# Kernel tuning notes

Hardware: AMD Instinct MI355X
Metric: run time of the kernel (lower is better)

Reference implementation:

```python
import jax, jax.numpy as jnp
import numpy as np

B, S, D, H = 2, 2048, 1024, 16
DK = D // H


def setup_inputs() -> dict:
    key = jax.random.key(0)
    ks = jax.random.split(key, 11)
    scale = 1.0 / np.sqrt(D)
    inp = {
        'q': jax.random.normal(ks[0], (B, S, D), jnp.float32),
        'k': jax.random.normal(ks[1], (B, S, D), jnp.float32),
        'v': jax.random.normal(ks[2], (B, S, D), jnp.float32),
        'mask': jnp.tril(jnp.ones((S, S), jnp.int32))[None, None],  # [1,1,S,S] causal
        'w_q': jax.random.normal(ks[3], (D, D), jnp.float32) * scale,
        'b_q': jax.random.normal(ks[4], (D,), jnp.float32) * scale,
        'w_k': jax.random.normal(ks[5], (D, D), jnp.float32) * scale,
        'b_k': jax.random.normal(ks[6], (D,), jnp.float32) * scale,
        'w_v': jax.random.normal(ks[7], (D, D), jnp.float32) * scale,
        'b_v': jax.random.normal(ks[8], (D,), jnp.float32) * scale,
        'w_o': jax.random.normal(ks[9], (D, D), jnp.float32) * scale,
        'b_o': jax.random.normal(ks[10], (D,), jnp.float32) * scale,
    }
    return inp


def reference(q, k, v, mask, w_q, b_q, w_k, b_k, w_v, b_v, w_o, b_o):
    # Linear projections (torch Linear: x @ W^T + b; here weights stored as [D_in, D_out])
    query = q @ w_q + b_q  # [B,S,D]
    key_ = k @ w_k + b_k
    value = v @ w_v + b_v
    # split heads -> [B,H,S,DK]
    def split(x):
        return x.reshape(B, S, H, DK).transpose(0, 2, 1, 3)
    qh, kh, vh = split(query), split(key_), split(value)
    scores = jnp.einsum('bhqd,bhkd->bhqk', qh, kh) / jnp.sqrt(jnp.float32(DK))
    scores = jnp.where(mask == 0, jnp.float32(-1e9), scores)
    attn = jax.nn.softmax(scores, axis=-1)  # dropout p=0.0 -> identity
    out = jnp.einsum('bhqk,bhkd->bhqd', attn, vh)  # [B,H,S,DK]
    out = out.transpose(0, 2, 1, 3).reshape(B, S, D)
    return out @ w_o + b_o
```

## Files before the change

kernel.cpp:

```cpp
#include <hip/hip_runtime.h>

typedef unsigned short u16;
typedef unsigned int u32;
typedef __attribute__((ext_vector_type(8))) short short8;
typedef __attribute__((ext_vector_type(4))) float f32x4;
typedef __attribute__((ext_vector_type(4))) float float4v;
typedef __attribute__((ext_vector_type(4))) u16 u16x4;
typedef __attribute__((ext_vector_type(2))) u32 u32x2;

#define DEV static __device__ __forceinline__

static constexpr int S_LEN = 2048;
static constexpr int D_MODEL = 1024;
static constexpr int N_HEADS = 16;
static constexpr int DK = 64;
static constexpr float LOG2E = 1.4426950408889634f;
static constexpr float SM_SHIFT = 12.0f;

#if defined(__has_builtin)
#if __has_builtin(__builtin_amdgcn_exp2f)
#define EXP2(x) __builtin_amdgcn_exp2f(x)
#else
#define EXP2(x) exp2f(x)
#endif
#else
#define EXP2(x) exp2f(x)
#endif

DEV u16 f2bf(float f) {
  u32 u = __builtin_bit_cast(u32, f);
  u32 r = (u + 0x7FFFu + ((u >> 16) & 1u)) >> 16;
  return (u16)r;
}

DEV u32 pk2bf(float lo, float hi) {
  u32 d;
  asm("v_cvt_pk_bf16_f32 %0, %1, %2" : "=v"(d) : "v"(lo), "v"(hi));
  return d;
}

DEV void async16(const void* g, void* l) {
  __builtin_amdgcn_global_load_lds(
      (const __attribute__((address_space(1))) u32*)g,
      (__attribute__((address_space(3))) u32*)l, 16, 0, 0);
}

DEV short8 lds_frag(const u16* tile, int row, int byteInRow) {
  const char* p = (const char*)tile + row * 128 + (byteInRow ^ ((row & 7) << 4));
  return *(const short8*)p;
}

DEV f32x4 mfma16(short8 a, short8 b, f32x4 c) {
  return __builtin_amdgcn_mfma_f32_16x16x32_bf16(a, b, c, 0, 0, 0);
}

__global__ void k_cvt3(const float* __restrict__ q, const float* __restrict__ k,
                       const float* __restrict__ v, u16* __restrict__ xq,
                       u16* __restrict__ xk, u16* __restrict__ xv, int n) {
  const float* src = blockIdx.y == 0 ? q : (blockIdx.y == 1 ? k : v);
  u16* dst = blockIdx.y == 0 ? xq : (blockIdx.y == 1 ? xk : xv);
  int i = (blockIdx.x * blockDim.x + threadIdx.x) * 4;
  int stride = gridDim.x * blockDim.x * 4;
  for (; i < n; i += stride) {
    float4v f = *(const float4v*)(src + i);
    u16x4 o;
    o[0] = f2bf(f[0]); o[1] = f2bf(f[1]); o[2] = f2bf(f[2]); o[3] = f2bf(f[3]);
    *(u16x4*)(dst + i) = o;
  }
}

__global__ void k_twz4(const float* __restrict__ wq, const float* __restrict__ wk,
                       const float* __restrict__ wv, const float* __restrict__ wo,
                       u16* __restrict__ tq, u16* __restrict__ tk,
                       u16* __restrict__ tv, u16* __restrict__ to_) {
  __shared__ u16 t[64][65];
  const int z = blockIdx.z;
  const float* W = z == 0 ? wq : (z == 1 ? wk : (z == 2 ? wv : wo));
  u16* Wt = z == 0 ? tq : (z == 1 ? tk : (z == 2 ? tv : to_));
  const int n0 = blockIdx.x * 64;
  const int k0 = blockIdx.y * 64;
  const int tid = threadIdx.x;
  const int c = tid & 63, r0 = tid >> 6;
#pragma unroll
  for (int j = 0; j < 16; ++j) {
    int r = r0 + j * 4;
    t[r][c] = f2bf(W[(size_t)(k0 + r) * D_MODEL + n0 + c]);
  }
  __syncthreads();
#pragma unroll
  for (int j = 0; j < 16; ++j) {
    int r = r0 + j * 4;
    Wt[(size_t)(n0 + r) * D_MODEL + k0 + c] = t[c][r];
  }
}

__global__ __launch_bounds__(256, 2) void k_gemm3(
    const u16* __restrict__ Xq, const u16* __restrict__ Xk, const u16* __restrict__ Xv,
    const u16* __restrict__ Wtq, const u16* __restrict__ Wtk, const u16* __restrict__ Wtv,
    const float* __restrict__ bq, const float* __restrict__ bk, const float* __restrict__ bv,
    u16* __restrict__ Qh, u16* __restrict__ Kh, u16* __restrict__ Vtp) {
  const int z = blockIdx.z;
  const u16* A = z == 0 ? Xq : (z == 1 ? Xk : Xv);
  const u16* Bt = z == 0 ? Wtq : (z == 1 ? Wtk : Wtv);
  const float* bias = z == 0 ? bq : (z == 1 ? bk : bv);
  u16* obf = z == 0 ? Qh : (z == 1 ? Kh : Vtp);
  const float scale = z == 0 ? 0.125f * LOG2E : 1.0f;

  __shared__ __align__(16) u16 As[128 * 64];
  __shared__ __align__(16) u16 Bs[128 * 64];
  const int tid = threadIdx.x;
  const int lane = tid & 63, w = tid >> 6;
  const int l15 = lane & 15, l4 = lane >> 4;
  const int bm = blockIdx.x * 128, bn = blockIdx.y * 128;
  const int wr = (w >> 1) * 64, wc = (w & 1) * 64;
  const int sr = tid >> 3, sc8 = tid & 7;
  f32x4 acc[4][4] = {};

  for (int k0 = 0; k0 < 1024; k0 += 64) {
    __syncthreads();
#pragma unroll
    for (int j = 0; j < 4; ++j) {
      int row = sr + j * 32;
      int col = (sc8 ^ (row & 7)) << 3;
      async16(A + (size_t)(bm + row) * 1024 + k0 + col, (char*)As + tid * 16 + j * 4096);
      async16(Bt + (size_t)(bn + row) * 1024 + k0 + col, (char*)Bs + tid * 16 + j * 4096);
    }
    __syncthreads();
    short8 af[4][2], bfv[4][2];
#pragma unroll
    for (int mi = 0; mi < 4; ++mi)
#pragma unroll
      for (int kk = 0; kk < 2; ++kk)
        af[mi][kk] = lds_frag(As, wr + mi * 16 + l15, kk * 64 + l4 * 16);
#pragma unroll
    for (int ni = 0; ni < 4; ++ni)
#pragma unroll
      for (int kk = 0; kk < 2; ++kk)
        bfv[ni][kk] = lds_frag(Bs, wc + ni * 16 + l15, kk * 64 + l4 * 16);
#pragma unroll
    for (int kk = 0; kk < 2; ++kk)
#pragma unroll
      for (int mi = 0; mi < 4; ++mi)
#pragma unroll
        for (int ni = 0; ni < 4; ++ni)
          acc[mi][ni] = mfma16(af[mi][kk], bfv[ni][kk], acc[mi][ni]);
  }

#pragma unroll
  for (int mi = 0; mi < 4; ++mi)
#pragma unroll
    for (int ni = 0; ni < 4; ++ni) {
      const int row0 = bm + wr + mi * 16 + l4 * 4;
      const int col = bn + wc + ni * 16 + l15;
      const int h = col >> 6, dk = col & 63;
      const int b = row0 >> 11, s0 = row0 & 2047;
      if (z == 2) {
        u16x4 pk;
#pragma unroll
        for (int r = 0; r < 4; ++r) pk[r] = f2bf(acc[mi][ni][r] + bias[col]);
        *(u16x4*)(obf + ((size_t)((b * N_HEADS + h) * DK + dk)) * S_LEN + s0) = pk;
      } else {
#pragma unroll
        for (int r = 0; r < 4; ++r) {
          float vv = (acc[mi][ni][r] + bias[col]) * scale;
          obf[(((size_t)(b * N_HEADS + h) * S_LEN + s0 + r) << 6) + dk] = f2bf(vv);
        }
      }
    }
}

__global__ __launch_bounds__(256, 2) void k_gemmO(
    const u16* __restrict__ A, const u16* __restrict__ Bt,
    const float* __restrict__ bias, float* __restrict__ ofp) {
  __shared__ __align__(16) u16 As[128 * 64];
  __shared__ __align__(16) u16 Bs[64 * 64];
  const int tid = threadIdx.x;
  const int lane = tid & 63, w = tid >> 6;
  const int l15 = lane & 15, l4 = lane >> 4;
  const int bm = blockIdx.x * 128, bn = blockIdx.y * 64;
  const int wr = w * 32;
  const int sr = tid >> 3, sc8 = tid & 7;
  f32x4 acc[2][4] = {};

  for (int k0 = 0; k0 < 1024; k0 += 64) {
    __syncthreads();
#pragma unroll
    for (int j = 0; j < 4; ++j) {
      int row = sr + j * 32;
      int col = (sc8 ^ (row & 7)) << 3;
      async16(A + (size_t)(bm + row) * 1024 + k0 + col, (char*)As + tid * 16 + j * 4096);
      if (j < 2)
        async16(Bt + (size_t)(bn + row) * 1024 + k0 + col, (char*)Bs + tid * 16 + j * 4096);
    }
    __syncthreads();
    short8 af[2][2], bfv[4][2];
#pragma unroll
    for (int mi = 0; mi < 2; ++mi)
#pragma unroll
      for (int kk = 0; kk < 2; ++kk)
        af[mi][kk] = lds_frag(As, wr + mi * 16 + l15, kk * 64 + l4 * 16);
#pragma unroll
    for (int ni = 0; ni < 4; ++ni)
#pragma unroll
      for (int kk = 0; kk < 2; ++kk)
        bfv[ni][kk] = lds_frag(Bs, ni * 16 + l15, kk * 64 + l4 * 16);
#pragma unroll
    for (int kk = 0; kk < 2; ++kk)
#pragma unroll
      for (int mi = 0; mi < 2; ++mi)
#pragma unroll
        for (int ni = 0; ni < 4; ++ni)
          acc[mi][ni] = mfma16(af[mi][kk], bfv[ni][kk], acc[mi][ni]);
  }

#pragma unroll
  for (int mi = 0; mi < 2; ++mi)
#pragma unroll
    for (int ni = 0; ni < 4; ++ni)
#pragma unroll
      for (int r = 0; r < 4; ++r) {
        int row = bm + wr + mi * 16 + l4 * 4 + r;
        int col = bn + ni * 16 + l15;
        ofp[(size_t)row * D_MODEL + col] = acc[mi][ni][r] + bias[col];
      }
}

__global__ __launch_bounds__(512, 6) void k_attn(
    const u16* __restrict__ Qh, const u16* __restrict__ Kh,
    const u16* __restrict__ Vt, u16* __restrict__ Om,
    float* __restrict__ Po, float* __restrict__ Pl) {
  __shared__ __align__(16) u16 Ks[2][64 * 64];
  __shared__ __align__(16) u16 Vs[2][64 * 64];
  __shared__ __align__(16) u16 Ps[8][16 * 64];
  const int tid = threadIdx.x;
  const int lane = tid & 63, w = tid >> 6;
  const int l15 = lane & 15, l4 = lane >> 4;
  const int bid = blockIdx.x;

  int bh, g, c, tbeg, tend;
  bool partial;
  if (bid < 256) {
    bh = bid & 31; g = 8 + (bid >> 5); c = 0; tbeg = 0; tend = 16; partial = true;
  } else if (bid < 512) {
    int i = bid - 256;
    bh = i & 31; g = 15 - (i >> 5); c = 1; tbeg = 16; tend = 2 * g + 2; partial = true;
  } else {
    int i = bid - 512;
    bh = i & 31; g = 7 - (i >> 5); c = 0; tbeg = 0; tend = 2 * g + 2; partial = false;
  }

  const u16* Qb = Qh + (size_t)bh * S_LEN * DK;
  const u16* Kb = Kh + (size_t)bh * S_LEN * DK;
  const u16* Vb = Vt + (size_t)bh * DK * S_LEN;
  const int q0 = g * 128;
  const int qw = q0 + w * 16;
  const int sc8 = tid & 7;
  u16* Pw = Ps[w];

  auto stage = [&](int t0, int buf) {
    int row = tid >> 3;
    int col = (sc8 ^ (row & 7)) << 3;
    async16(Kb + (size_t)(t0 + row) * DK + col, (char*)Ks[buf] + tid * 16);
    async16(Vb + (size_t)row * S_LEN + t0 + col, (char*)Vs[buf] + tid * 16);
  };

  short8 qf[2];
#pragma unroll
  for (int kk = 0; kk < 2; ++kk)
    qf[kk] = *(const short8*)(Qb + (size_t)(qw + l15) * DK + kk * 32 + l4 * 8);

  f32x4 o[4] = {};
  float rs = 0.f;

  stage(tbeg << 6, 0);
  __syncthreads();
  int cur = 0;
#pragma unroll 1
  for (int ti = tbeg; ti < tend; ++ti) {
    const int t0 = ti << 6;
    if (ti + 1 < tend) stage((ti + 1) << 6, cur ^ 1);

    f32x4 sf[4];
#pragma unroll
    for (int mi = 0; mi < 4; ++mi)
#pragma unroll
      for (int r = 0; r < 4; ++r) sf[mi][r] = -SM_SHIFT;
    __builtin_amdgcn_s_setprio(1);
#pragma unroll
    for (int kk = 0; kk < 2; ++kk)
#pragma unroll
      for (int mi = 0; mi < 4; ++mi) {
        short8 kf = lds_frag(Ks[cur], mi * 16 + l15, kk * 64 + l4 * 16);
        sf[mi] = mfma16(kf, qf[kk], sf[mi]);
      }
    __builtin_amdgcn_s_setprio(0);

    if (t0 + 63 > qw) {
      const int qrow = qw + l15;
#pragma unroll
      for (int mi = 0; mi < 4; ++mi)
#pragma unroll
        for (int r = 0; r < 4; ++r)
          if (t0 + mi * 16 + l4 * 4 + r > qrow) sf[mi][r] = -1e30f;
    }

#pragma unroll
    for (int mi = 0; mi < 4; ++mi) {
      float p0 = EXP2(sf[mi][0]);
      float p1 = EXP2(sf[mi][1]);
      float p2 = EXP2(sf[mi][2]);
      float p3 = EXP2(sf[mi][3]);
      rs += (p0 + p1) + (p2 + p3);
      u32x2 pk;
      pk[0] = pk2bf(p0, p1);
      pk[1] = pk2bf(p2, p3);
      *(u32x2*)((char*)Pw + l15 * 128 + ((mi * 32 + l4 * 8) ^ ((l15 & 7) << 4))) = pk;
    }

    __builtin_amdgcn_s_setprio(1);
#pragma unroll
    for (int kk = 0; kk < 2; ++kk) {
      short8 pf = lds_frag(Pw, l15, kk * 64 + l4 * 16);
#pragma unroll
      for (int ni = 0; ni < 4; ++ni) {
        short8 vf = lds_frag(Vs[cur], ni * 16 + l15, kk * 64 + l4 * 16);
        o[ni] = mfma16(pf, vf, o[ni]);
      }
    }
    __builtin_amdgcn_s_setprio(0);
    __syncthreads();
    cur ^= 1;
  }

  rs += __shfl_xor(rs, 16);
  rs += __shfl_xor(rs, 32);

  if (partial) {
    const int slot = ((bh << 3) + (g - 8)) * 2 + c;
    float* PoS = Po + (size_t)slot * (128 * 64);
#pragma unroll
    for (int ni = 0; ni < 4; ++ni)
#pragma unroll
      for (int r = 0; r < 4; ++r)
        PoS[(w * 16 + l4 * 4 + r) * 64 + ni * 16 + l15] = o[ni][r];
    if (l4 == 0) Pl[slot * 128 + w * 16 + l15] = rs;
  } else {
    f32x4 lv;
#pragma unroll
    for (int r = 0; r < 4; ++r) lv[r] = __shfl(rs, l4 * 4 + r);
    const int b = bh >> 4, h = bh & 15;
#pragma unroll
    for (int ni = 0; ni < 4; ++ni)
#pragma unroll
      for (int r = 0; r < 4; ++r) {
        int s = qw + l4 * 4 + r;
        int d = ni * 16 + l15;
        Om[(size_t)(b * S_LEN + s) * D_MODEL + h * DK + d] = f2bf(o[ni][r] / lv[r]);
      }
  }
}

__global__ void k_comb(const float* __restrict__ Po, const float* __restrict__ Pl,
                       u16* __restrict__ Om) {
  const int bh = blockIdx.x, g8 = blockIdx.y;
  const int tid = threadIdx.x;
  const int slot0 = ((bh << 3) + g8) * 2;
  const float* P0 = Po + (size_t)slot0 * (128 * 64);
  const float* P1 = P0 + (128 * 64);
  const float* L0 = Pl + slot0 * 128;
  const float* L1 = L0 + 128;
  const int b = bh >> 4, h = bh & 15;
  const int row0 = tid >> 4, c4 = (tid & 15) * 4;
#pragma unroll
  for (int j = 0; j < 8; ++j) {
    int row = j * 16 + row0;
    float4v a = *(const float4v*)(P0 + row * 64 + c4);
    float4v bb = *(const float4v*)(P1 + row * 64 + c4);
    float inv = 1.f / (L0[row] + L1[row]);
    u16x4 ov;
#pragma unroll
    for (int i = 0; i < 4; ++i) ov[i] = f2bf((a[i] + bb[i]) * inv);
    int s = 1024 + g8 * 128 + row;
    *(u16x4*)(Om + (size_t)(b * S_LEN + s) * D_MODEL + h * DK + c4) = ov;
  }
}

extern "C" void kernel_launch(void* const* d_in, const int* in_sizes, int n_in,
                              void* d_out, int out_size, void* d_ws, size_t ws_size,
                              hipStream_t stream) {
  (void)in_sizes; (void)n_in; (void)out_size; (void)ws_size;
  const float* q  = (const float*)d_in[0];
  const float* k  = (const float*)d_in[1];
  const float* v  = (const float*)d_in[2];
  const float* wq = (const float*)d_in[4];
  const float* bq = (const float*)d_in[5];
  const float* wk = (const float*)d_in[6];
  const float* bk = (const float*)d_in[7];
  const float* wv = (const float*)d_in[8];
  const float* bv = (const float*)d_in[9];
  const float* wo = (const float*)d_in[10];
  const float* bo = (const float*)d_in[11];
  float* out = (float*)d_out;

  char* ws = (char*)d_ws;
  const size_t XB = (size_t)4096 * 1024 * 2;
  const size_t WB = (size_t)1024 * 1024 * 2;
  u16* Xq  = (u16*)(ws);
  u16* Xk  = (u16*)(ws + XB);
  u16* Xv  = (u16*)(ws + 2 * XB);
  u16* Wtq = (u16*)(ws + 3 * XB);
  u16* Wtk = (u16*)(ws + 3 * XB + WB);
  u16* Wtv = (u16*)(ws + 3 * XB + 2 * WB);
  u16* Wto = (u16*)(ws + 3 * XB + 3 * WB);
  u16* Qh  = (u16*)(ws + 3 * XB + 4 * WB);
  u16* Kh  = (u16*)(ws + 4 * XB + 4 * WB);
  u16* Vtp = (u16*)(ws + 5 * XB + 4 * WB);
  float* Po = (float*)(ws + XB);
  float* Pl = (float*)(ws + 6 * XB + 4 * WB);
  u16* Om  = Xq;

  const int n = 4096 * 1024;
  k_cvt3<<<dim3(512, 3), 256, 0, stream>>>(q, k, v, Xq, Xk, Xv, n);
  k_twz4<<<dim3(16, 16, 4), 256, 0, stream>>>(wq, wk, wv, wo, Wtq, Wtk, Wtv, Wto);
  k_gemm3<<<dim3(32, 8, 3), 256, 0, stream>>>(Xq, Xk, Xv, Wtq, Wtk, Wtv,
                                              bq, bk, bv, Qh, Kh, Vtp);
  k_attn<<<768, 512, 0, stream>>>(Qh, Kh, Vtp, Om, Po, Pl);
  k_comb<<<dim3(32, 8), 256, 0, stream>>>(Po, Pl, Om);
  k_gemmO<<<dim3(32, 16), 256, 0, stream>>>(Om, Wto, bo, out);
}
```

Measured before the change: 111.8 us.

## Switch attention to 32x32 MFMA with register-resident P via permlane swap

The attention kernel now computes QK^T and PV with 32x32x16 bf16 MFMAs, each wave owning 32 query rows, and the block drops to 4 waves. The softmax probabilities stay in registers and are rearranged into the B-operand layout with v_permlane32_swap instead of going through a per-wave LDS scratch buffer. The goal is fewer LDS round trips and fewer MFMA/LDS instructions per tile, plus vectorized output stores. In exchange the kernel holds more registers per wave and runs half as many waves per block.

```diff
diff --git a/kernel.cpp b/kernel.cpp
--- a/kernel.cpp
+++ b/kernel.cpp
@@ -4,6 +4,7 @@
 typedef unsigned int u32;
 typedef __attribute__((ext_vector_type(8))) short short8;
 typedef __attribute__((ext_vector_type(4))) float f32x4;
+typedef __attribute__((ext_vector_type(16))) float f32x16;
 typedef __attribute__((ext_vector_type(4))) float float4v;
 typedef __attribute__((ext_vector_type(4))) u16 u16x4;
 typedef __attribute__((ext_vector_type(2))) u32 u32x2;
@@ -39,6 +40,16 @@
   return d;
 }
 
+DEV void swap32(u32& a, u32& b) {
+  asm volatile("v_permlane32_swap_b32 %0, %1" : "+v"(a), "+v"(b));
+}
+
+DEV short8 mk8(u32 w0, u32 w1, u32 w2, u32 w3) {
+  union { u32 u[4]; short8 s; } t;
+  t.u[0] = w0; t.u[1] = w1; t.u[2] = w2; t.u[3] = w3;
+  return t.s;
+}
+
 DEV void async16(const void* g, void* l) {
   __builtin_amdgcn_global_load_lds(
       (const __attribute__((address_space(1))) u32*)g,
@@ -52,6 +63,10 @@
 
 DEV f32x4 mfma16(short8 a, short8 b, f32x4 c) {
   return __builtin_amdgcn_mfma_f32_16x16x32_bf16(a, b, c, 0, 0, 0);
+}
+
+DEV f32x16 mfma32(short8 a, short8 b, f32x16 c) {
+  return __builtin_amdgcn_mfma_f32_32x32x16_bf16(a, b, c, 0, 0, 0);
 }
 
 __global__ void k_cvt3(const float* __restrict__ q, const float* __restrict__ k,
@@ -225,16 +240,15 @@
       }
 }
 
-__global__ __launch_bounds__(512, 6) void k_attn(
+__global__ __launch_bounds__(256, 3) void k_attn(
     const u16* __restrict__ Qh, const u16* __restrict__ Kh,
     const u16* __restrict__ Vt, u16* __restrict__ Om,
     float* __restrict__ Po, float* __restrict__ Pl) {
   __shared__ __align__(16) u16 Ks[2][64 * 64];
   __shared__ __align__(16) u16 Vs[2][64 * 64];
-  __shared__ __align__(16) u16 Ps[8][16 * 64];
   const int tid = threadIdx.x;
   const int lane = tid & 63, w = tid >> 6;
-  const int l15 = lane & 15, l4 = lane >> 4;
+  const int l31 = lane & 31, hf = lane >> 5;
   const int bid = blockIdx.x;
 
   int bh, g, c, tbeg, tend;
@@ -253,23 +267,25 @@
   const u16* Kb = Kh + (size_t)bh * S_LEN * DK;
   const u16* Vb = Vt + (size_t)bh * DK * S_LEN;
   const int q0 = g * 128;
-  const int qw = q0 + w * 16;
+  const int qw = q0 + w * 32;
   const int sc8 = tid & 7;
-  u16* Pw = Ps[w];
 
   auto stage = [&](int t0, int buf) {
-    int row = tid >> 3;
-    int col = (sc8 ^ (row & 7)) << 3;
-    async16(Kb + (size_t)(t0 + row) * DK + col, (char*)Ks[buf] + tid * 16);
-    async16(Vb + (size_t)row * S_LEN + t0 + col, (char*)Vs[buf] + tid * 16);
+#pragma unroll
+    for (int j = 0; j < 2; ++j) {
+      int row = (tid >> 3) + j * 32;
+      int col = (sc8 ^ (row & 7)) << 3;
+      async16(Kb + (size_t)(t0 + row) * DK + col, (char*)Ks[buf] + tid * 16 + j * 4096);
+      async16(Vb + (size_t)row * S_LEN + t0 + col, (char*)Vs[buf] + tid * 16 + j * 4096);
+    }
   };
 
-  short8 qf[2];
-#pragma unroll
-  for (int kk = 0; kk < 2; ++kk)
-    qf[kk] = *(const short8*)(Qb + (size_t)(qw + l15) * DK + kk * 32 + l4 * 8);
-
-  f32x4 o[4] = {};
+  short8 qB[4];
+#pragma unroll
+  for (int cc = 0; cc < 4; ++cc)
+    qB[cc] = *(const short8*)(Qb + (size_t)(qw + l31) * DK + cc * 16 + hf * 8);
+
+  f32x16 od0 = {}, od1 = {};
   float rs = 0.f;
 
   stage(tbeg << 6, 0);
@@ -280,83 +296,110 @@
     const int t0 = ti << 6;
     if (ti + 1 < tend) stage((ti + 1) << 6, cur ^ 1);
 
-    f32x4 sf[4];
-#pragma unroll
-    for (int mi = 0; mi < 4; ++mi)
-#pragma unroll
-      for (int r = 0; r < 4; ++r) sf[mi][r] = -SM_SHIFT;
+    f32x16 s0, s1;
+#pragma unroll
+    for (int r = 0; r < 16; ++r) { s0[r] = -SM_SHIFT; s1[r] = -SM_SHIFT; }
     __builtin_amdgcn_s_setprio(1);
 #pragma unroll
-    for (int kk = 0; kk < 2; ++kk)
-#pragma unroll
-      for (int mi = 0; mi < 4; ++mi) {
-        short8 kf = lds_frag(Ks[cur], mi * 16 + l15, kk * 64 + l4 * 16);
-        sf[mi] = mfma16(kf, qf[kk], sf[mi]);
+    for (int cc = 0; cc < 4; ++cc) {
+      short8 k0f = lds_frag(Ks[cur], l31, cc * 32 + hf * 16);
+      short8 k1f = lds_frag(Ks[cur], 32 + l31, cc * 32 + hf * 16);
+      s0 = mfma32(k0f, qB[cc], s0);
+      s1 = mfma32(k1f, qB[cc], s1);
+    }
+    __builtin_amdgcn_s_setprio(0);
+
+    if (t0 + 63 > qw) {
+      const int qrow = qw + l31;
+#pragma unroll
+      for (int r = 0; r < 16; ++r) {
+        int kr = t0 + ((r & 3) + 8 * (r >> 2) + 4 * hf);
+        if (kr > qrow) s0[r] = -1e30f;
+        if (kr + 32 > qrow) s1[r] = -1e30f;
       }
-    __builtin_amdgcn_s_setprio(0);
-
-    if (t0 + 63 > qw) {
-      const int qrow = qw + l15;
-#pragma unroll
-      for (int mi = 0; mi < 4; ++mi)
-#pragma unroll
-        for (int r = 0; r < 4; ++r)
-          if (t0 + mi * 16 + l4 * 4 + r > qrow) sf[mi][r] = -1e30f;
-    }
-
-#pragma unroll
-    for (int mi = 0; mi < 4; ++mi) {
-      float p0 = EXP2(sf[mi][0]);
-      float p1 = EXP2(sf[mi][1]);
-      float p2 = EXP2(sf[mi][2]);
-      float p3 = EXP2(sf[mi][3]);
-      rs += (p0 + p1) + (p2 + p3);
-      u32x2 pk;
-      pk[0] = pk2bf(p0, p1);
-      pk[1] = pk2bf(p2, p3);
-      *(u32x2*)((char*)Pw + l15 * 128 + ((mi * 32 + l4 * 8) ^ ((l15 & 7) << 4))) = pk;
-    }
+    }
+
+    float rs0 = 0.f, rs1 = 0.f;
+#pragma unroll
+    for (int r = 0; r < 16; ++r) {
+      s0[r] = EXP2(s0[r]);
+      s1[r] = EXP2(s1[r]);
+      rs0 += s0[r];
+      rs1 += s1[r];
+    }
+    rs += rs0 + rs1;
+
+    u32 a0 = pk2bf(s0[0], s0[1]), b0 = pk2bf(s0[4], s0[5]);
+    u32 c0 = pk2bf(s0[2], s0[3]), d0 = pk2bf(s0[6], s0[7]);
+    swap32(a0, b0); swap32(c0, d0);
+    short8 pb00 = mk8(a0, c0, b0, d0);
+    u32 e0 = pk2bf(s0[8], s0[9]), f0 = pk2bf(s0[12], s0[13]);
+    u32 g0 = pk2bf(s0[10], s0[11]), h0 = pk2bf(s0[14], s0[15]);
+    swap32(e0, f0); swap32(g0, h0);
+    short8 pb01 = mk8(e0, g0, f0, h0);
+    u32 a1 = pk2bf(s1[0], s1[1]), b1 = pk2bf(s1[4], s1[5]);
+    u32 c1 = pk2bf(s1[2], s1[3]), d1 = pk2bf(s1[6], s1[7]);
+    swap32(a1, b1); swap32(c1, d1);
+    short8 pb10 = mk8(a1, c1, b1, d1);
+    u32 e1 = pk2bf(s1[8], s1[9]), f1 = pk2bf(s1[12], s1[13]);
+    u32 g1 = pk2bf(s1[10], s1[11]), h1 = pk2bf(s1[14], s1[15]);
+    swap32(e1, f1); swap32(g1, h1);
+    short8 pb11 = mk8(e1, g1, f1, h1);
 
     __builtin_amdgcn_s_setprio(1);
-#pragma unroll
-    for (int kk = 0; kk < 2; ++kk) {
-      short8 pf = lds_frag(Pw, l15, kk * 64 + l4 * 16);
-#pragma unroll
-      for (int ni = 0; ni < 4; ++ni) {
-        short8 vf = lds_frag(Vs[cur], ni * 16 + l15, kk * 64 + l4 * 16);
-        o[ni] = mfma16(pf, vf, o[ni]);
-      }
+    {
+      short8 v00 = lds_frag(Vs[cur], l31, hf * 16);
+      short8 v10 = lds_frag(Vs[cur], 32 + l31, hf * 16);
+      od0 = mfma32(v00, pb00, od0);
+      od1 = mfma32(v10, pb00, od1);
+      short8 v01 = lds_frag(Vs[cur], l31, 32 + hf * 16);
+      short8 v11 = lds_frag(Vs[cur], 32 + l31, 32 + hf * 16);
+      od0 = mfma32(v01, pb01, od0);
+      od1 = mfma32(v11, pb01, od1);
+      short8 v02 = lds_frag(Vs[cur], l31, 64 + hf * 16);
+      short8 v12 = lds_frag(Vs[cur], 32 + l31, 64 + hf * 16);
+      od0 = mfma32(v02, pb10, od0);
+      od1 = mfma32(v12, pb10, od1);
+      short8 v03 = lds_frag(Vs[cur], l31, 96 + hf * 16);
+      short8 v13 = lds_frag(Vs[cur], 32 + l31, 96 + hf * 16);
+      od0 = mfma32(v03, pb11, od0);
+      od1 = mfma32(v13, pb11, od1);
     }
     __builtin_amdgcn_s_setprio(0);
     __syncthreads();
     cur ^= 1;
   }
 
-  rs += __shfl_xor(rs, 16);
   rs += __shfl_xor(rs, 32);
 
+  const int qloc = w * 32 + l31;
   if (partial) {
     const int slot = ((bh << 3) + (g - 8)) * 2 + c;
     float* PoS = Po + (size_t)slot * (128 * 64);
 #pragma unroll
-    for (int ni = 0; ni < 4; ++ni)
-#pragma unroll
-      for (int r = 0; r < 4; ++r)
-        PoS[(w * 16 + l4 * 4 + r) * 64 + ni * 16 + l15] = o[ni][r];
-    if (l4 == 0) Pl[slot * 128 + w * 16 + l15] = rs;
+    for (int rr = 0; rr < 4; ++rr) {
+      float4v v0, v1;
+#pragma unroll
+      for (int i = 0; i < 4; ++i) { v0[i] = od0[rr * 4 + i]; v1[i] = od1[rr * 4 + i]; }
+      *(float4v*)(PoS + qloc * 64 + rr * 8 + 4 * hf) = v0;
+      *(float4v*)(PoS + qloc * 64 + 32 + rr * 8 + 4 * hf) = v1;
+    }
+    if (hf == 0) Pl[slot * 128 + qloc] = rs;
   } else {
-    f32x4 lv;
-#pragma unroll
-    for (int r = 0; r < 4; ++r) lv[r] = __shfl(rs, l4 * 4 + r);
-    const int b = bh >> 4, h = bh & 15;
-#pragma unroll
-    for (int ni = 0; ni < 4; ++ni)
-#pragma unroll
-      for (int r = 0; r < 4; ++r) {
-        int s = qw + l4 * 4 + r;
-        int d = ni * 16 + l15;
-        Om[(size_t)(b * S_LEN + s) * D_MODEL + h * DK + d] = f2bf(o[ni][r] / lv[r]);
+    const float inv = 1.f / rs;
+    const int b = bh >> 4, hd = bh & 15;
+    u16* dst = Om + (size_t)(b * S_LEN + qw + l31) * D_MODEL + hd * DK;
+#pragma unroll
+    for (int rr = 0; rr < 4; ++rr) {
+      u16x4 o0, o1;
+#pragma unroll
+      for (int i = 0; i < 4; ++i) {
+        o0[i] = f2bf(od0[rr * 4 + i] * inv);
+        o1[i] = f2bf(od1[rr * 4 + i] * inv);
       }
+      *(u16x4*)(dst + rr * 8 + 4 * hf) = o0;
+      *(u16x4*)(dst + 32 + rr * 8 + 4 * hf) = o1;
+    }
   }
 }
 
@@ -424,7 +467,7 @@
   k_twz4<<<dim3(16, 16, 4), 256, 0, stream>>>(wq, wk, wv, wo, Wtq, Wtk, Wtv, Wto);
   k_gemm3<<<dim3(32, 8, 3), 256, 0, stream>>>(Xq, Xk, Xv, Wtq, Wtk, Wtv,
                                               bq, bk, bv, Qh, Kh, Vtp);
-  k_attn<<<768, 512, 0, stream>>>(Qh, Kh, Vtp, Om, Po, Pl);
+  k_attn<<<768, 256, 0, stream>>>(Qh, Kh, Vtp, Om, Po, Pl);
   k_comb<<<dim3(32, 8), 256, 0, stream>>>(Po, Pl, Om);
   k_gemmO<<<dim3(32, 16), 256, 0, stream>>>(Om, Wto, bo, out);
 }
```

Result: no change. 112.4 us (+0.5%).
